# Optimization experiments

Hardware: AMD Instinct MI355X
Metric: run time of the kernel (lower is better)

Reference implementation:

```python
import jax, jax.numpy as jnp
import numpy as np

N_HEADS = 8


def setup_inputs() -> dict:
    key = jax.random.key(0)
    ks = jax.random.split(key, 12)
    B, C, H, W = 16, 256, 64, 64
    std = 1.0 / np.sqrt(C)  # init_std(conv) ~ 1/sqrt(fan_in) for a 1x1 conv
    return {
        "x": jax.random.normal(ks[0], (B, C, H, W), jnp.float32),
        "mod_multiplier": jax.random.normal(ks[1], (B, C), jnp.float32),
        "mod_bias": jax.random.normal(ks[2], (B, C), jnp.float32),
        "qkv_w": jax.random.normal(ks[3], (3 * C, C), jnp.float32) * std,
        "qkv_b": jnp.zeros((3 * C,), jnp.float32),
        "pe_q_h": jax.random.normal(ks[4], (1, C, H, 1), jnp.float32) * 0.02,
        "pe_q_w": jax.random.normal(ks[5], (1, C, 1, W), jnp.float32) * 0.02,
        "pe_k_h": jax.random.normal(ks[6], (1, C, H, 1), jnp.float32) * 0.02,
        "pe_k_w": jax.random.normal(ks[7], (1, C, 1, W), jnp.float32) * 0.02,
        "pre_act_bias": jnp.zeros((1, C, 1, 1), jnp.float32),
        "pre_qkv_bias": jnp.zeros((1, C, 1, 1), jnp.float32),
    }


def reference(x, mod_multiplier, mod_bias, qkv_w, qkv_b, pe_q_h, pe_q_w, pe_k_h, pe_k_w, pre_act_bias, pre_qkv_bias):
    B, C, H, W = x.shape
    hs = C // N_HEADS  # head_size
    dot_scale = jnp.asarray(hs, x.dtype) ** 0.5

    x_preact = jax.nn.silu(x + pre_act_bias)
    # 1x1 conv == channel GEMM: [B,C,H,W] x [3C,C] -> [B,3C,H,W]
    qkv = jnp.einsum('bchw,oc->bohw', x_preact + pre_qkv_bias, qkv_w) + qkv_b[None, :, None, None]
    q, k, v = jnp.split(qkv, 3, axis=1)

    q = q + pe_q_h + pe_q_w
    k = k + pe_k_h + pe_k_w
    q = q * mod_multiplier[:, :, None, None] + mod_bias[:, :, None, None]

    # view as [B, n_heads, head_size, H*W]
    q = q.reshape(B, N_HEADS, hs, H * W)
    k = k.reshape(B, N_HEADS, hs, H * W)
    v = v.reshape(B, N_HEADS, hs, H * W)

    # channel-attention: logits [B, n_heads, hs, hs]
    logits = jnp.einsum('bhcn,bhdn->bhcd', q, k) / dot_scale
    weights = jax.nn.softmax(logits, axis=-1)
    out = jnp.einsum('bhcd,bhdn->bhcn', weights, v).reshape(B, C, H, W)

    return jnp.concatenate((x_preact, out), axis=1)
```

## Files before the change

kernel.cpp:

```cpp
#include <hip/hip_runtime.h>

typedef short bf16x8 __attribute__((ext_vector_type(8)));
typedef float f32x4 __attribute__((ext_vector_type(4)));

__device__ __forceinline__ float b2f(unsigned short u) {
  union { unsigned int i; float f; } v; v.i = ((unsigned int)u) << 16; return v.f;
}
__device__ __forceinline__ unsigned short f2b(float f) {
  unsigned int u = __float_as_uint(f);
  u += 0x7fffu + ((u >> 16) & 1u);
  return (unsigned short)(u >> 16);
}
__device__ __forceinline__ float silu_f(float s) { return s / (1.0f + __expf(-s)); }

__device__ __forceinline__ void split2(float f, unsigned short& h, unsigned short& l) {
  h = f2b(f);
  l = f2b(f - b2f(h));
}

__device__ __forceinline__ void gload16(const unsigned short* g, unsigned short* l) {
  __builtin_amdgcn_global_load_lds(
      (const __attribute__((address_space(1))) unsigned int*)g,
      (__attribute__((address_space(3))) unsigned int*)l, 16, 0, 0);
}

__device__ __forceinline__ void unpack8(const unsigned* p, bf16x8& hi, bf16x8& lo) {
  uint4 a = *(const uint4*)p;
  uint4 b = *(const uint4*)(p + 4);
  unsigned u[8] = {a.x, a.y, a.z, a.w, b.x, b.y, b.z, b.w};
  unsigned hw[4], lw[4];
  #pragma unroll
  for (int j = 0; j < 4; j++) {
    hw[j] = __builtin_amdgcn_perm(u[2 * j + 1], u[2 * j], 0x05040100u);
    lw[j] = __builtin_amdgcn_perm(u[2 * j + 1], u[2 * j], 0x07060302u);
  }
  hi = *(bf16x8*)hw;
  lo = *(bf16x8*)lw;
}

__global__ __launch_bounds__(256) void k_wsplit(
    const float* __restrict__ W, unsigned short* __restrict__ Wh,
    unsigned short* __restrict__ Wl) {
  int e = (blockIdx.x * 256 + threadIdx.x) * 8;
  float4 a = *(const float4*)(W + e);
  float4 b = *(const float4*)(W + e + 4);
  float v[8] = {a.x, a.y, a.z, a.w, b.x, b.y, b.z, b.w};
  unsigned short h[8], l[8];
  #pragma unroll
  for (int j = 0; j < 8; j++) split2(v[j], h[j], l[j]);
  uint4 ph, pl;
  ph.x = h[0] | ((unsigned)h[1] << 16); ph.y = h[2] | ((unsigned)h[3] << 16);
  ph.z = h[4] | ((unsigned)h[5] << 16); ph.w = h[6] | ((unsigned)h[7] << 16);
  pl.x = l[0] | ((unsigned)l[1] << 16); pl.y = l[2] | ((unsigned)l[3] << 16);
  pl.z = l[4] | ((unsigned)l[5] << 16); pl.w = l[6] | ((unsigned)l[7] << 16);
  *(uint4*)(Wh + e) = ph;
  *(uint4*)(Wl + e) = pl;
}

__global__ __launch_bounds__(256) void k_prep(
    const float* __restrict__ x, const float* __restrict__ pab,
    const float* __restrict__ pqb, float* __restrict__ out) {
  __shared__ unsigned short th[64 * 64], tl[64 * 64];
  int blk = blockIdx.x;
  int nb = blk & 63;
  int cb = (blk >> 6) & 3;
  int b = blk >> 8;
  int n0 = nb * 64, c0 = cb * 64;
  int t = threadIdx.x;
  int nn = (t & 15) * 4;
  #pragma unroll
  for (int p = 0; p < 2; p++) {
    int c = 2 * (p * 16 + (t >> 4));
    float pa0 = pab[c0 + c], pq0 = pqb[c0 + c];
    float pa1 = pab[c0 + c + 1], pq1 = pqb[c0 + c + 1];
    float4 x0 = *(const float4*)(x + ((long long)(b * 256 + c0 + c)) * 4096 + n0 + nn);
    float4 x1 = *(const float4*)(x + ((long long)(b * 256 + c0 + c + 1)) * 4096 + n0 + nn);
    float s0[4] = {silu_f(x0.x + pa0), silu_f(x0.y + pa0),
                   silu_f(x0.z + pa0), silu_f(x0.w + pa0)};
    float s1[4] = {silu_f(x1.x + pa1), silu_f(x1.y + pa1),
                   silu_f(x1.z + pa1), silu_f(x1.w + pa1)};
    float4 sv0 = {s0[0], s0[1], s0[2], s0[3]};
    float4 sv1 = {s1[0], s1[1], s1[2], s1[3]};
    *(float4*)(out + ((long long)(b * 512 + c0 + c)) * 4096 + n0 + nn) = sv0;
    *(float4*)(out + ((long long)(b * 512 + c0 + c + 1)) * 4096 + n0 + nn) = sv1;
    float t0[4] = {s0[0] + pq0, s0[1] + pq0, s0[2] + pq0, s0[3] + pq0};
    float t1[4] = {s1[0] + pq1, s1[1] + pq1, s1[2] + pq1, s1[3] + pq1};
    #pragma unroll
    for (int j = 0; j < 4; j++) {
      int nr = nn + j;
      unsigned short h0, l0, h1, l1;
      split2(t0[j], h0, l0);
      split2(t1[j], h1, l1);
      int pcol = ((((c >> 3) ^ (nr & 7)) << 3) | (c & 7));
      *(unsigned int*)(th + nr * 64 + pcol) = (unsigned)h0 | ((unsigned)h1 << 16);
      *(unsigned int*)(tl + nr * 64 + pcol) = (unsigned)l0 | ((unsigned)l1 << 16);
    }
  }
  __syncthreads();
  unsigned short* Th = (unsigned short*)(out + ((long long)(b * 512 + 256)) * 4096);
  unsigned short* Tl = Th + 4096 * 256;
  #pragma unroll
  for (int q = 0; q < 2; q++) {
    int s = q * 256 + t;
    int n = s >> 3, sc = s & 7;
    int psc = sc ^ (n & 7);
    uint4 vh = *(const uint4*)(th + n * 64 + psc * 8);
    uint4 vl = *(const uint4*)(tl + n * 64 + psc * 8);
    *(uint4*)(Th + (long long)(n0 + n) * 256 + c0 + sc * 8) = vh;
    *(uint4*)(Tl + (long long)(n0 + n) * 256 + c0 + sc * 8) = vl;
  }
}

__global__ __launch_bounds__(256, 3) void k_qkl(
    const unsigned short* __restrict__ Wh, const unsigned short* __restrict__ Wl,
    const float* __restrict__ qkvb,
    const float* __restrict__ peqh, const float* __restrict__ peqw,
    const float* __restrict__ pekh, const float* __restrict__ pekw,
    const float* __restrict__ modm, const float* __restrict__ modb,
    const float* __restrict__ outT, float* __restrict__ kv,
    float* __restrict__ logits) {
  __shared__ __align__(16) unsigned char smem[32768];
  unsigned short* stg = (unsigned short*)smem;
  unsigned* qk = (unsigned*)smem;
  float* red = (float*)smem;

  int bx = blockIdx.x;
  int ntile = bx & 31, h = (bx >> 5) & 7, b = bx >> 8;
  int n0 = ntile * 128;
  int t = threadIdx.x, lane = t & 63, w = t >> 6;
  int l15 = lane & 15, l4 = lane >> 4;

  const unsigned short* Th =
      (const unsigned short*)(outT + ((long long)(b * 512 + 256)) * 4096);
  const unsigned short* Tl = Th + 4096 * 256;

  const unsigned short* csrc[7];
  unsigned short* cdst[7];
  int nc = (w < 2) ? 7 : 6;
  int lrow = lane >> 2;
  int lslot = ((lane & 3) ^ ((lane >> 3) & 3)) * 8;
  #pragma unroll
  for (int i = 0; i < 7; i++) {
    int c = w + 4 * i;
    if (c > 25) c = 25;
    const unsigned short* plane;
    int rowb, ldsoff;
    if (c < 4) {
      plane = Wh; rowb = ((c & 2) ? 256 : 0) + h * 32 + (c & 1) * 16;
      ldsoff = c * 512;
    } else if (c < 8) {
      int s2 = c - 4;
      plane = Wl; rowb = ((s2 & 2) ? 256 : 0) + h * 32 + (s2 & 1) * 16;
      ldsoff = c * 512;
    } else if (c < 10) {
      plane = Wh; rowb = 512 + h * 32 + (c - 8) * 16;
      ldsoff = 4096 + (c - 8) * 512;
    } else if (c < 18) {
      plane = Th; rowb = n0 + (c - 10) * 16;
      ldsoff = 5120 + (c - 10) * 512;
    } else {
      plane = Tl; rowb = n0 + (c - 18) * 16;
      ldsoff = 9216 + (c - 18) * 512;
    }
    csrc[i] = plane + (long long)(rowb + lrow) * 256 + lslot;
    cdst[i] = stg + ldsoff;
  }

  int sw = (l4 ^ ((l15 >> 1) & 3)) << 3;
  f32x4 z = {0.f, 0.f, 0.f, 0.f};
  f32x4 acc[4][2];
  f32x4 accv[2][2];
  #pragma unroll
  for (int i = 0; i < 4; i++)
    #pragma unroll
    for (int j = 0; j < 2; j++) acc[i][j] = z;
  #pragma unroll
  for (int i = 0; i < 2; i++)
    #pragma unroll
    for (int j = 0; j < 2; j++) accv[i][j] = z;

  for (int step = 0; step < 8; ++step) {
    int k0 = step * 32;
    #pragma unroll
    for (int i = 0; i < 7; i++)
      if (i < nc) gload16(csrc[i] + k0, cdst[i]);
    __syncthreads();
    bf16x8 bh[2], av[2];
    #pragma unroll
    for (int j = 0; j < 2; j++)
      bh[j] = *(const bf16x8*)(stg + 5120 + (w * 32 + j * 16 + l15) * 32 + sw);
    #pragma unroll
    for (int i = 0; i < 2; i++)
      av[i] = *(const bf16x8*)(stg + 4096 + (i * 16 + l15) * 32 + sw);
    #pragma unroll
    for (int i = 0; i < 2; i++)
      #pragma unroll
      for (int j = 0; j < 2; j++)
        accv[i][j] = __builtin_amdgcn_mfma_f32_16x16x32_bf16(av[i], bh[j], accv[i][j], 0, 0, 0);
    __builtin_amdgcn_sched_barrier(0);
    bf16x8 ah[4], al[4], bl[2];
    #pragma unroll
    for (int i = 0; i < 4; i++) {
      int ro = (i * 16 + l15) * 32 + sw;
      ah[i] = *(const bf16x8*)(stg + ro);
      al[i] = *(const bf16x8*)(stg + 2048 + ro);
    }
    #pragma unroll
    for (int j = 0; j < 2; j++)
      bl[j] = *(const bf16x8*)(stg + 9216 + (w * 32 + j * 16 + l15) * 32 + sw);
    #pragma unroll
    for (int i = 0; i < 4; i++)
      #pragma unroll
      for (int j = 0; j < 2; j++) {
        acc[i][j] = __builtin_amdgcn_mfma_f32_16x16x32_bf16(ah[i], bh[j], acc[i][j], 0, 0, 0);
        acc[i][j] = __builtin_amdgcn_mfma_f32_16x16x32_bf16(ah[i], bl[j], acc[i][j], 0, 0, 0);
        acc[i][j] = __builtin_amdgcn_mfma_f32_16x16x32_bf16(al[i], bh[j], acc[i][j], 0, 0, 0);
      }
    __syncthreads();
  }

  int b256 = b * 256;
  #pragma unroll
  for (int i = 0; i < 2; i++) {
    #pragma unroll
    for (int r = 0; r < 4; r++) {
      int row = i * 16 + l4 * 4 + r;
      int cch = h * 32 + row;
      float bias = qkvb[512 + cch];
      #pragma unroll
      for (int j = 0; j < 2; j++) {
        int n = n0 + w * 32 + j * 16 + l15;
        kv[((long long)(b256 + cch)) * 4096 + n] = accv[i][j][r] + bias;
      }
    }
  }

  #pragma unroll
  for (int i = 0; i < 4; i++) {
    #pragma unroll
    for (int r = 0; r < 4; r++) {
      int row = i * 16 + l4 * 4 + r;
      int cch = h * 32 + (row & 31);
      float bias = qkvb[(row & 32) ? (256 + cch) : cch];
      float mm = 0.f, mb = 0.f;
      if (row < 32) { mm = modm[b256 + cch]; mb = modb[b256 + cch]; }
      #pragma unroll
      for (int j = 0; j < 2; j++) {
        int nl = w * 32 + j * 16 + l15;
        int n = n0 + nl;
        int hh = n >> 6, ww = n & 63;
        float v = acc[i][j][r] + bias;
        if (row < 32) {
          v += peqh[cch * 64 + hh] + peqw[cch * 64 + ww];
          v = v * mm + mb;
        } else {
          v += pekh[cch * 64 + hh] + pekw[cch * 64 + ww];
        }
        unsigned short hi_, lo_;
        split2(v, hi_, lo_);
        int pch = (nl >> 3) ^ (row & 15);
        qk[row * 128 + pch * 8 + (nl & 7)] = (unsigned)hi_ | ((unsigned)lo_ << 16);
      }
    }
  }
  __syncthreads();

  f32x4 acc2[2][2] = {z, z, z, z};
  int chn = w * 4 + l4;
  bf16x8 qh[2], ql[2], kh[2], kl[2];
  #pragma unroll
  for (int i2 = 0; i2 < 2; i2++) {
    int row = i2 * 16 + l15;
    unpack8(qk + row * 128 + ((chn ^ l15) << 3), qh[i2], ql[i2]);
    unpack8(qk + (row + 32) * 128 + ((chn ^ l15) << 3), kh[i2], kl[i2]);
  }
  acc2[0][0] = __builtin_amdgcn_mfma_f32_16x16x32_bf16(qh[0], kh[0], acc2[0][0], 0, 0, 0);
  acc2[0][0] = __builtin_amdgcn_mfma_f32_16x16x32_bf16(qh[0], kl[0], acc2[0][0], 0, 0, 0);
  acc2[0][0] = __builtin_amdgcn_mfma_f32_16x16x32_bf16(ql[0], kh[0], acc2[0][0], 0, 0, 0);
  acc2[0][1] = __builtin_amdgcn_mfma_f32_16x16x32_bf16(qh[0], kh[1], acc2[0][1], 0, 0, 0);
  acc2[0][1] = __builtin_amdgcn_mfma_f32_16x16x32_bf16(qh[0], kl[1], acc2[0][1], 0, 0, 0);
  acc2[0][1] = __builtin_amdgcn_mfma_f32_16x16x32_bf16(ql[0], kh[1], acc2[0][1], 0, 0, 0);
  acc2[1][0] = __builtin_amdgcn_mfma_f32_16x16x32_bf16(qh[1], kh[0], acc2[1][0], 0, 0, 0);
  acc2[1][0] = __builtin_amdgcn_mfma_f32_16x16x32_bf16(qh[1], kl[0], acc2[1][0], 0, 0, 0);
  acc2[1][0] = __builtin_amdgcn_mfma_f32_16x16x32_bf16(ql[1], kh[0], acc2[1][0], 0, 0, 0);
  acc2[1][1] = __builtin_amdgcn_mfma_f32_16x16x32_bf16(qh[1], kh[1], acc2[1][1], 0, 0, 0);
  acc2[1][1] = __builtin_amdgcn_mfma_f32_16x16x32_bf16(qh[1], kl[1], acc2[1][1], 0, 0, 0);
  acc2[1][1] = __builtin_amdgcn_mfma_f32_16x16x32_bf16(ql[1], kh[1], acc2[1][1], 0, 0, 0);

  __syncthreads();
  #pragma unroll
  for (int i2 = 0; i2 < 2; i2++)
    #pragma unroll
    for (int j2 = 0; j2 < 2; j2++)
      #pragma unroll
      for (int r = 0; r < 4; r++)
        red[w * 1024 + (i2 * 16 + l4 * 4 + r) * 32 + j2 * 16 + l15] = acc2[i2][j2][r];
  __syncthreads();
  const float scale = 0.1767766952966369f;
  int bhid = b * 8 + h;
  #pragma unroll
  for (int i = 0; i < 4; i++) {
    int idx = i * 256 + t;
    float s = (red[idx] + red[1024 + idx] + red[2048 + idx] + red[3072 + idx]) * scale;
    atomicAdd(logits + (long long)bhid * 1024 + idx, s);
  }
}

__global__ __launch_bounds__(256) void k_pv(
    const float* __restrict__ kv,
    const float* __restrict__ logits,
    float* __restrict__ out) {
  int bx = blockIdx.x;
  int ntile = bx & 15, bh = bx >> 4;
  int b = bh >> 3, h = bh & 7;
  int t = threadIdx.x;
  __shared__ float raw[32][33];
  __shared__ float wsm[32][33];
  #pragma unroll
  for (int i = 0; i < 4; i++) {
    int idx = i * 256 + t;
    raw[idx >> 5][idx & 31] = logits[(long long)bh * 1024 + idx];
  }
  __syncthreads();
  if (t < 32) {
    float mx = -1e30f;
    for (int d = 0; d < 32; d++) mx = fmaxf(mx, raw[t][d]);
    float e[32]; float s = 0.f;
    for (int d = 0; d < 32; d++) { e[d] = __expf(raw[t][d] - mx); s += e[d]; }
    float inv = 1.0f / s;
    for (int d = 0; d < 32; d++) wsm[t][d] = e[d] * inv;
  }
  __syncthreads();
  int rg = t >> 6;
  int nl = (t & 63) * 4;
  int n0 = ntile * 256 + nl;
  const float* vb = kv + ((long long)(b * 256 + h * 32)) * 4096 + n0;
  float acc[8][4];
  #pragma unroll
  for (int r = 0; r < 8; r++)
    #pragma unroll
    for (int i = 0; i < 4; i++) acc[r][i] = 0.f;
  for (int d = 0; d < 32; d++) {
    float4 vv = *(const float4*)(vb + (long long)d * 4096);
    #pragma unroll
    for (int r = 0; r < 8; r++) {
      float wv = wsm[rg * 8 + r][d];
      acc[r][0] += wv * vv.x; acc[r][1] += wv * vv.y;
      acc[r][2] += wv * vv.z; acc[r][3] += wv * vv.w;
    }
  }
  #pragma unroll
  for (int r = 0; r < 8; r++) {
    long long oidx = ((long long)(b * 512 + 256 + h * 32 + rg * 8 + r)) * 4096 + n0;
    float4 ov = {acc[r][0], acc[r][1], acc[r][2], acc[r][3]};
    *(float4*)(out + oidx) = ov;
  }
}

extern "C" void kernel_launch(void* const* d_in, const int* in_sizes, int n_in,
                              void* d_out, int out_size, void* d_ws, size_t ws_size,
                              hipStream_t stream) {
  const float* x    = (const float*)d_in[0];
  const float* modm = (const float*)d_in[1];
  const float* modb = (const float*)d_in[2];
  const float* Wq   = (const float*)d_in[3];
  const float* qkvb = (const float*)d_in[4];
  const float* peqh = (const float*)d_in[5];
  const float* peqw = (const float*)d_in[6];
  const float* pekh = (const float*)d_in[7];
  const float* pekw = (const float*)d_in[8];
  const float* pab  = (const float*)d_in[9];
  const float* pqb  = (const float*)d_in[10];
  float* out = (float*)d_out;

  unsigned short* Wh = (unsigned short*)d_ws;
  unsigned short* Wl = Wh + 768 * 256;
  float* logits = (float*)((char*)d_ws + (1 << 20));
  float* kv = (float*)((char*)d_ws + 3 * (1 << 20));

  hipMemsetAsync(logits, 0, 16 * 8 * 32 * 32 * sizeof(float), stream);
  k_wsplit<<<96, 256, 0, stream>>>(Wq, Wh, Wl);
  k_prep<<<4096, 256, 0, stream>>>(x, pab, pqb, out);
  k_qkl<<<4096, 256, 0, stream>>>(Wh, Wl, qkvb, peqh, peqw, pekh, pekw,
                                  modm, modb, out, kv, logits);
  k_pv<<<2048, 256, 0, stream>>>(kv, logits, out);
}
```

Measured before the change: 317.6 us.

## Pre-swizzle weights into MFMA fragment order and load directly from global

The weight hi/lo split kernel is folded into the prep kernel, which now writes the weights already in per-lane MFMA fragment order. The QK GEMM then loads A fragments straight from global memory into registers instead of staging them through LDS, cutting LDS staging traffic and per-step copy instructions. The kernel launch count drops by one. The prep transpose moves to a 32-bit word XOR swizzle, and the qk and reduction LDS buffers get padded strides to avoid bank conflicts, at the cost of a slightly larger LDS footprint and more global loads per step.

After: 324.0 us. Within noise of the previous version (+2.0%).

```diff
diff --git a/kernel.cpp b/kernel.cpp
--- a/kernel.cpp
+++ b/kernel.cpp
@@ -38,30 +38,51 @@
   lo = *(bf16x8*)lw;
 }
 
-__global__ __launch_bounds__(256) void k_wsplit(
-    const float* __restrict__ W, unsigned short* __restrict__ Wh,
-    unsigned short* __restrict__ Wl) {
-  int e = (blockIdx.x * 256 + threadIdx.x) * 8;
-  float4 a = *(const float4*)(W + e);
-  float4 b = *(const float4*)(W + e + 4);
-  float v[8] = {a.x, a.y, a.z, a.w, b.x, b.y, b.z, b.w};
-  unsigned short h[8], l[8];
-  #pragma unroll
-  for (int j = 0; j < 8; j++) split2(v[j], h[j], l[j]);
-  uint4 ph, pl;
-  ph.x = h[0] | ((unsigned)h[1] << 16); ph.y = h[2] | ((unsigned)h[3] << 16);
-  ph.z = h[4] | ((unsigned)h[5] << 16); ph.w = h[6] | ((unsigned)h[7] << 16);
-  pl.x = l[0] | ((unsigned)l[1] << 16); pl.y = l[2] | ((unsigned)l[3] << 16);
-  pl.z = l[4] | ((unsigned)l[5] << 16); pl.w = l[6] | ((unsigned)l[7] << 16);
-  *(uint4*)(Wh + e) = ph;
-  *(uint4*)(Wl + e) = pl;
-}
-
 __global__ __launch_bounds__(256) void k_prep(
     const float* __restrict__ x, const float* __restrict__ pab,
-    const float* __restrict__ pqb, float* __restrict__ out) {
-  __shared__ unsigned short th[64 * 64], tl[64 * 64];
+    const float* __restrict__ pqb, const float* __restrict__ W,
+    unsigned short* __restrict__ Wfq, unsigned short* __restrict__ Wfl,
+    unsigned short* __restrict__ Wfv, float* __restrict__ out) {
+  __shared__ unsigned th2[64 * 32], tl2[64 * 32];
   int blk = blockIdx.x;
+  if (blk < 96) {
+    int u = blk * 256 + threadIdx.x;
+    int lane = u & 63, l15 = lane & 15, l4 = lane >> 4;
+    int row, k;
+    unsigned short* dh;
+    unsigned short* dl = nullptr;
+    if (u < 16384) {
+      int i = (u >> 6) & 3, step = (u >> 8) & 7, hh = u >> 11;
+      row = (i < 2) ? (hh * 32 + i * 16 + l15) : (256 + hh * 32 + (i - 2) * 16 + l15);
+      k = step * 32 + l4 * 8;
+      dh = Wfq + (long long)u * 8;
+      dl = Wfl + (long long)u * 8;
+    } else {
+      int u2 = u - 16384;
+      int i2 = (u2 >> 6) & 1, step = (u2 >> 7) & 7, hh = u2 >> 10;
+      row = 512 + hh * 32 + i2 * 16 + l15;
+      k = step * 32 + l4 * 8;
+      dh = Wfv + (long long)u2 * 8;
+    }
+    float4 a = *(const float4*)(W + row * 256 + k);
+    float4 bq = *(const float4*)(W + row * 256 + k + 4);
+    float v[8] = {a.x, a.y, a.z, a.w, bq.x, bq.y, bq.z, bq.w};
+    unsigned short h8[8], l8[8];
+    #pragma unroll
+    for (int j = 0; j < 8; j++) split2(v[j], h8[j], l8[j]);
+    uint4 ph;
+    ph.x = h8[0] | ((unsigned)h8[1] << 16); ph.y = h8[2] | ((unsigned)h8[3] << 16);
+    ph.z = h8[4] | ((unsigned)h8[5] << 16); ph.w = h8[6] | ((unsigned)h8[7] << 16);
+    *(uint4*)dh = ph;
+    if (dl) {
+      uint4 pl;
+      pl.x = l8[0] | ((unsigned)l8[1] << 16); pl.y = l8[2] | ((unsigned)l8[3] << 16);
+      pl.z = l8[4] | ((unsigned)l8[5] << 16); pl.w = l8[6] | ((unsigned)l8[7] << 16);
+      *(uint4*)dl = pl;
+    }
+    return;
+  }
+  blk -= 96;
   int nb = blk & 63;
   int cb = (blk >> 6) & 3;
   int b = blk >> 8;
@@ -70,7 +91,8 @@
   int nn = (t & 15) * 4;
   #pragma unroll
   for (int p = 0; p < 2; p++) {
-    int c = 2 * (p * 16 + (t >> 4));
+    int cp = p * 16 + (t >> 4);
+    int c = 2 * cp;
     float pa0 = pab[c0 + c], pq0 = pqb[c0 + c];
     float pa1 = pab[c0 + c + 1], pq1 = pqb[c0 + c + 1];
     float4 x0 = *(const float4*)(x + ((long long)(b * 256 + c0 + c)) * 4096 + n0 + nn);
@@ -91,9 +113,9 @@
       unsigned short h0, l0, h1, l1;
       split2(t0[j], h0, l0);
       split2(t1[j], h1, l1);
-      int pcol = ((((c >> 3) ^ (nr & 7)) << 3) | (c & 7));
-      *(unsigned int*)(th + nr * 64 + pcol) = (unsigned)h0 | ((unsigned)h1 << 16);
-      *(unsigned int*)(tl + nr * 64 + pcol) = (unsigned)l0 | ((unsigned)l1 << 16);
+      int pidx = nr * 32 + (cp ^ (nr & 31));
+      th2[pidx] = (unsigned)h0 | ((unsigned)h1 << 16);
+      tl2[pidx] = (unsigned)l0 | ((unsigned)l1 << 16);
     }
   }
   __syncthreads();
@@ -103,23 +125,30 @@
   for (int q = 0; q < 2; q++) {
     int s = q * 256 + t;
     int n = s >> 3, sc = s & 7;
-    int psc = sc ^ (n & 7);
-    uint4 vh = *(const uint4*)(th + n * 64 + psc * 8);
-    uint4 vl = *(const uint4*)(tl + n * 64 + psc * 8);
+    unsigned wh[4], wl[4];
+    #pragma unroll
+    for (int j = 0; j < 4; j++) {
+      int pidx = n * 32 + ((sc * 4 + j) ^ (n & 31));
+      wh[j] = th2[pidx];
+      wl[j] = tl2[pidx];
+    }
+    uint4 vh = {wh[0], wh[1], wh[2], wh[3]};
+    uint4 vl = {wl[0], wl[1], wl[2], wl[3]};
     *(uint4*)(Th + (long long)(n0 + n) * 256 + c0 + sc * 8) = vh;
     *(uint4*)(Tl + (long long)(n0 + n) * 256 + c0 + sc * 8) = vl;
   }
 }
 
 __global__ __launch_bounds__(256, 3) void k_qkl(
-    const unsigned short* __restrict__ Wh, const unsigned short* __restrict__ Wl,
+    const unsigned short* __restrict__ Wfq, const unsigned short* __restrict__ Wfl,
+    const unsigned short* __restrict__ Wfv,
     const float* __restrict__ qkvb,
     const float* __restrict__ peqh, const float* __restrict__ peqw,
     const float* __restrict__ pekh, const float* __restrict__ pekw,
     const float* __restrict__ modm, const float* __restrict__ modb,
     const float* __restrict__ outT, float* __restrict__ kv,
     float* __restrict__ logits) {
-  __shared__ __align__(16) unsigned char smem[32768];
+  __shared__ __align__(16) unsigned char smem[33792];
   unsigned short* stg = (unsigned short*)smem;
   unsigned* qk = (unsigned*)smem;
   float* red = (float*)smem;
@@ -134,37 +163,22 @@
       (const unsigned short*)(outT + ((long long)(b * 512 + 256)) * 4096);
   const unsigned short* Tl = Th + 4096 * 256;
 
-  const unsigned short* csrc[7];
-  unsigned short* cdst[7];
-  int nc = (w < 2) ? 7 : 6;
+  const unsigned short* csrc[4];
+  unsigned short* cdst[4];
   int lrow = lane >> 2;
   int lslot = ((lane & 3) ^ ((lane >> 3) & 3)) * 8;
   #pragma unroll
-  for (int i = 0; i < 7; i++) {
+  for (int i = 0; i < 4; i++) {
     int c = w + 4 * i;
-    if (c > 25) c = 25;
-    const unsigned short* plane;
-    int rowb, ldsoff;
-    if (c < 4) {
-      plane = Wh; rowb = ((c & 2) ? 256 : 0) + h * 32 + (c & 1) * 16;
-      ldsoff = c * 512;
-    } else if (c < 8) {
-      int s2 = c - 4;
-      plane = Wl; rowb = ((s2 & 2) ? 256 : 0) + h * 32 + (s2 & 1) * 16;
-      ldsoff = c * 512;
-    } else if (c < 10) {
-      plane = Wh; rowb = 512 + h * 32 + (c - 8) * 16;
-      ldsoff = 4096 + (c - 8) * 512;
-    } else if (c < 18) {
-      plane = Th; rowb = n0 + (c - 10) * 16;
-      ldsoff = 5120 + (c - 10) * 512;
-    } else {
-      plane = Tl; rowb = n0 + (c - 18) * 16;
-      ldsoff = 9216 + (c - 18) * 512;
-    }
+    const unsigned short* plane = (c < 8) ? Th : Tl;
+    int rowb = n0 + (c & 7) * 16;
     csrc[i] = plane + (long long)(rowb + lrow) * 256 + lslot;
-    cdst[i] = stg + ldsoff;
-  }
+    cdst[i] = stg + c * 512;
+  }
+
+  const unsigned short* aqb = Wfq + (long long)(h * 32) * 512 + lane * 8;
+  const unsigned short* alb = Wfl + (long long)(h * 32) * 512 + lane * 8;
+  const unsigned short* avb = Wfv + (long long)(h * 16) * 512 + lane * 8;
 
   int sw = (l4 ^ ((l15 >> 1) & 3)) << 3;
   f32x4 z = {0.f, 0.f, 0.f, 0.f};
@@ -182,39 +196,36 @@
   for (int step = 0; step < 8; ++step) {
     int k0 = step * 32;
     #pragma unroll
-    for (int i = 0; i < 7; i++)
-      if (i < nc) gload16(csrc[i] + k0, cdst[i]);
+    for (int i = 0; i < 4; i++) gload16(csrc[i] + k0, cdst[i]);
+    bf16x8 ah[4], alo[4], av[2];
+    #pragma unroll
+    for (int i = 0; i < 4; i++) {
+      ah[i]  = *(const bf16x8*)(aqb + (step * 4 + i) * 512);
+      alo[i] = *(const bf16x8*)(alb + (step * 4 + i) * 512);
+    }
+    #pragma unroll
+    for (int i = 0; i < 2; i++)
+      av[i] = *(const bf16x8*)(avb + (step * 2 + i) * 512);
     __syncthreads();
-    bf16x8 bh[2], av[2];
-    #pragma unroll
-    for (int j = 0; j < 2; j++)
-      bh[j] = *(const bf16x8*)(stg + 5120 + (w * 32 + j * 16 + l15) * 32 + sw);
-    #pragma unroll
-    for (int i = 0; i < 2; i++)
-      av[i] = *(const bf16x8*)(stg + 4096 + (i * 16 + l15) * 32 + sw);
+    bf16x8 bh[2], bl[2];
+    #pragma unroll
+    for (int j = 0; j < 2; j++) {
+      int ro = (w * 32 + j * 16 + l15) * 32 + sw;
+      bh[j] = *(const bf16x8*)(stg + ro);
+      bl[j] = *(const bf16x8*)(stg + 4096 + ro);
+    }
     #pragma unroll
     for (int i = 0; i < 2; i++)
       #pragma unroll
       for (int j = 0; j < 2; j++)
         accv[i][j] = __builtin_amdgcn_mfma_f32_16x16x32_bf16(av[i], bh[j], accv[i][j], 0, 0, 0);
-    __builtin_amdgcn_sched_barrier(0);
-    bf16x8 ah[4], al[4], bl[2];
-    #pragma unroll
-    for (int i = 0; i < 4; i++) {
-      int ro = (i * 16 + l15) * 32 + sw;
-      ah[i] = *(const bf16x8*)(stg + ro);
-      al[i] = *(const bf16x8*)(stg + 2048 + ro);
-    }
-    #pragma unroll
-    for (int j = 0; j < 2; j++)
-      bl[j] = *(const bf16x8*)(stg + 9216 + (w * 32 + j * 16 + l15) * 32 + sw);
     #pragma unroll
     for (int i = 0; i < 4; i++)
       #pragma unroll
       for (int j = 0; j < 2; j++) {
         acc[i][j] = __builtin_amdgcn_mfma_f32_16x16x32_bf16(ah[i], bh[j], acc[i][j], 0, 0, 0);
         acc[i][j] = __builtin_amdgcn_mfma_f32_16x16x32_bf16(ah[i], bl[j], acc[i][j], 0, 0, 0);
-        acc[i][j] = __builtin_amdgcn_mfma_f32_16x16x32_bf16(al[i], bh[j], acc[i][j], 0, 0, 0);
+        acc[i][j] = __builtin_amdgcn_mfma_f32_16x16x32_bf16(alo[i], bh[j], acc[i][j], 0, 0, 0);
       }
     __syncthreads();
   }
@@ -259,7 +270,7 @@
         unsigned short hi_, lo_;
         split2(v, hi_, lo_);
         int pch = (nl >> 3) ^ (row & 15);
-        qk[row * 128 + pch * 8 + (nl & 7)] = (unsigned)hi_ | ((unsigned)lo_ << 16);
+        qk[row * 132 + pch * 8 + (nl & 7)] = (unsigned)hi_ | ((unsigned)lo_ << 16);
       }
     }
   }
@@ -271,8 +282,8 @@
   #pragma unroll
   for (int i2 = 0; i2 < 2; i2++) {
     int row = i2 * 16 + l15;
-    unpack8(qk + row * 128 + ((chn ^ l15) << 3), qh[i2], ql[i2]);
-    unpack8(qk + (row + 32) * 128 + ((chn ^ l15) << 3), kh[i2], kl[i2]);
+    unpack8(qk + row * 132 + ((chn ^ l15) << 3), qh[i2], ql[i2]);
+    unpack8(qk + (row + 32) * 132 + ((chn ^ l15) << 3), kh[i2], kl[i2]);
   }
   acc2[0][0] = __builtin_amdgcn_mfma_f32_16x16x32_bf16(qh[0], kh[0], acc2[0][0], 0, 0, 0);
   acc2[0][0] = __builtin_amdgcn_mfma_f32_16x16x32_bf16(qh[0], kl[0], acc2[0][0], 0, 0, 0);
@@ -294,14 +305,16 @@
     for (int j2 = 0; j2 < 2; j2++)
       #pragma unroll
       for (int r = 0; r < 4; r++)
-        red[w * 1024 + (i2 * 16 + l4 * 4 + r) * 32 + j2 * 16 + l15] = acc2[i2][j2][r];
+        red[w * 1056 + (i2 * 16 + l4 * 4 + r) * 33 + j2 * 16 + l15] = acc2[i2][j2][r];
   __syncthreads();
   const float scale = 0.1767766952966369f;
   int bhid = b * 8 + h;
   #pragma unroll
   for (int i = 0; i < 4; i++) {
     int idx = i * 256 + t;
-    float s = (red[idx] + red[1024 + idx] + red[2048 + idx] + red[3072 + idx]) * scale;
+    int crow = idx >> 5, dcol = idx & 31;
+    int ro = crow * 33 + dcol;
+    float s = (red[ro] + red[1056 + ro] + red[2112 + ro] + red[3168 + ro]) * scale;
     atomicAdd(logits + (long long)bhid * 1024 + idx, s);
   }
 }
@@ -373,15 +386,15 @@
   const float* pqb  = (const float*)d_in[10];
   float* out = (float*)d_out;
 
-  unsigned short* Wh = (unsigned short*)d_ws;
-  unsigned short* Wl = Wh + 768 * 256;
+  unsigned short* Wfq = (unsigned short*)d_ws;
+  unsigned short* Wfl = Wfq + 131072;
+  unsigned short* Wfv = Wfl + 131072;
   float* logits = (float*)((char*)d_ws + (1 << 20));
   float* kv = (float*)((char*)d_ws + 3 * (1 << 20));
 
   hipMemsetAsync(logits, 0, 16 * 8 * 32 * 32 * sizeof(float), stream);
-  k_wsplit<<<96, 256, 0, stream>>>(Wq, Wh, Wl);
-  k_prep<<<4096, 256, 0, stream>>>(x, pab, pqb, out);
-  k_qkl<<<4096, 256, 0, stream>>>(Wh, Wl, qkvb, peqh, peqw, pekh, pekw,
+  k_prep<<<4192, 256, 0, stream>>>(x, pab, pqb, Wq, Wfq, Wfl, Wfv, out);
+  k_qkl<<<4096, 256, 0, stream>>>(Wfq, Wfl, Wfv, qkvb, peqh, peqw, pekh, pekw,
                                   modm, modb, out, kv, logits);
   k_pv<<<2048, 256, 0, stream>>>(kv, logits, out);
 }
```
